# Kernel tuning notes

Measured on AMD Instinct MI355X. Metric: run time of the kernel, lower is better.

Reference implementation:

```python
import jax, jax.numpy as jnp
import numpy as np

D_EMBED = 32


def setup_inputs() -> dict:
    key = jax.random.key(0)
    ks = jax.random.split(key, 10)
    B, N, D = 16, 16384, D_EMBED
    s = 1.0 / np.sqrt(D)
    return {
        "h_pos": jax.random.normal(ks[0], (B, N, D), dtype=jnp.float32),
        "h_geo": jax.random.normal(ks[1], (B, N, D), dtype=jnp.float32),
        "n_clusters": 128,
        "Wq": jax.random.uniform(ks[2], (D, D), jnp.float32, -s, s),
        "bq": jax.random.uniform(ks[3], (D,), jnp.float32, -s, s),
        "Wk": jax.random.uniform(ks[4], (D, D), jnp.float32, -s, s),
        "bk": jax.random.uniform(ks[5], (D,), jnp.float32, -s, s),
        "Wv": jax.random.uniform(ks[6], (D, D), jnp.float32, -s, s),
        "bv": jax.random.uniform(ks[7], (D,), jnp.float32, -s, s),
        "Wo": jax.random.uniform(ks[8], (D, D), jnp.float32, -s, s),
        "bo": jax.random.uniform(ks[9], (D,), jnp.float32, -s, s),
    }


def reference(h_pos, h_geo, n_clusters, Wq, bq, Wk, bk, Wv, bv, Wo, bo):
    B, N, D = h_pos.shape
    C = n_clusters
    S = N // C  # cluster size (contiguous equal-size kmeans clusters)
    # Linear projections (torch Linear: x @ W^T + b)
    Q = h_geo @ Wq.T + bq
    K = h_geo @ Wk.T + bk
    V = h_pos @ Wv.T + bv
    # group points into clusters: [B, C, S, D]
    Qc = Q.reshape(B, C, S, D) * (1.0 / jnp.sqrt(jnp.asarray(D, Q.dtype)))
    Kc = K.reshape(B, C, S, D)
    Vc = V.reshape(B, C, S, D)
    # per-cluster attention: softmax(Q_c K_c^T) V_c
    scores = jnp.einsum("bcsd,bctd->bcst", Qc, Kc)  # [B, C, S, S]
    attn = jax.nn.softmax(scores, axis=-1)
    out = jnp.einsum("bcst,bctd->bcsd", attn, Vc).reshape(B, N, D)
    return out @ Wo.T + bo
```

## Files before the change

### kernel.cpp

```cpp
#include <hip/hip_runtime.h>

typedef __attribute__((ext_vector_type(4))) float  f32x4;
typedef __attribute__((ext_vector_type(8))) short  s16x8;

static __device__ __forceinline__ short f2bf(float x) {
    union { __bf16 b; short s; } u; u.b = (__bf16)x;
    return u.s;
}

static __device__ __forceinline__ s16x8 load_frag_f32(const float* __restrict__ base,
                                                      int stride, int row, int k0) {
    const float* p = base + (size_t)row * stride + k0;
    f32x4 a = *(const f32x4*)p;
    f32x4 b = *(const f32x4*)(p + 4);
    s16x8 f;
    f[0]=f2bf(a[0]); f[1]=f2bf(a[1]); f[2]=f2bf(a[2]); f[3]=f2bf(a[3]);
    f[4]=f2bf(b[0]); f[5]=f2bf(b[1]); f[6]=f2bf(b[2]); f[7]=f2bf(b[3]);
    return f;
}

#define MFMA(a,b,c) __builtin_amdgcn_mfma_f32_16x16x32_bf16((a),(b),(c),0,0,0)

#define GSCALE 0.25503164217809464f

__global__ __launch_bounds__(256, 3) void dlsa_kernel(
    const float* __restrict__ h_pos, const float* __restrict__ h_geo,
    const float* __restrict__ Wq, const float* __restrict__ bq,
    const float* __restrict__ Wk,
    const float* __restrict__ Wv, const float* __restrict__ bv,
    const float* __restrict__ Wo, const float* __restrict__ bo,
    float* __restrict__ out)
{
    constexpr int D = 32, S = 128, XS = 40;

    __shared__ __align__(16) short buf[20480];
    short* sVt = buf;
    short* sP  = buf + 4096;
    short* sXp = sP;
    float* cbuf = (float*)(buf + 9216);

    const int tid = threadIdx.x;
    const int wv  = tid >> 6;
    const int ln  = tid & 63;
    const int lr  = ln & 15;
    const int lg  = ln >> 4;
    const int lk  = lg << 3;
    const int r0  = wv * 32;

    short* gsl = buf + 9472 + wv * 1088;
    short* wsl = gsl + 1024;

    const f32x4 z4 = {0.f, 0.f, 0.f, 0.f};

    int cl0 = blockIdx.x * 2;
    s16x8 aXg[2], aXp[2];
    {
        const float* xg = h_geo + (size_t)cl0 * S * D;
        const float* xp = h_pos + (size_t)cl0 * S * D;
#pragma unroll
        for (int mi = 0; mi < 2; ++mi) {
            aXg[mi] = load_frag_f32(xg, D, r0 + mi * 16 + lr, lk);
            aXp[mi] = load_frag_f32(xp, D, r0 + mi * 16 + lr, lk);
        }
    }

    s16x8 aWq[2], bWk[2], a_bq;
#pragma unroll
    for (int ni = 0; ni < 2; ++ni) {
#pragma unroll
        for (int j = 0; j < 8; ++j) {
            aWq[ni][j] = f2bf(Wq[(lk + j) * 32 + ni * 16 + lr]);
            bWk[ni][j] = f2bf(Wk[(lk + j) * 32 + ni * 16 + lr]);
        }
    }
#pragma unroll
    for (int j = 0; j < 8; ++j) a_bq[j] = f2bf(bq[lk + j]);

#pragma unroll
    for (int ni = 0; ni < 2; ++ni)
#pragma unroll
        for (int kt = 0; kt < 2; ++kt) {
            f32x4 g = MFMA(aWq[ni], bWk[kt], z4);
#pragma unroll
            for (int r = 0; r < 4; ++r)
                gsl[(ni * 16 + lg * 4 + r) * 32 + kt * 16 + lr] = f2bf(g[r] * GSCALE);
        }
#pragma unroll
    for (int kt = 0; kt < 2; ++kt) {
        f32x4 w4 = MFMA(a_bq, bWk[kt], z4);
        if (lg == 0) wsl[kt * 16 + lr] = f2bf(w4[0] * GSCALE);
    }
    s16x8 fG[2];
#pragma unroll
    for (int ni = 0; ni < 2; ++ni)
        fG[ni] = *(const s16x8*)&gsl[(ni * 16 + lr) * 32 + lk];
    s16x8 wf = *(const s16x8*)&wsl[lk];
    if (lr != 0) {
#pragma unroll
        for (int i = 0; i < 8; ++i) wf[i] = 0;
    }
    s16x8 fWv[2], fWo[2];
    float vbv[2], vbo[2];
#pragma unroll
    for (int ni = 0; ni < 2; ++ni) {
        int n = ni * 16 + lr;
        fWv[ni] = load_frag_f32(Wv, 32, n, lk);
        fWo[ni] = load_frag_f32(Wo, 32, n, lk);
        vbv[ni] = bv[n]; vbo[ni] = bo[n];
    }

#pragma unroll
    for (int it = 0; it < 2; ++it) {
        float* outp = out + (size_t)(cl0 + it) * S * D;
        if (it) __syncthreads();

#pragma unroll
        for (int mi = 0; mi < 2; ++mi) {
            f32x4 cc = MFMA(aXg[mi], wf, z4);
            if (lr == 0) {
#pragma unroll
                for (int r = 0; r < 4; ++r) cbuf[r0 + mi * 16 + lg * 4 + r] = cc[r];
            }
#pragma unroll
            for (int ni = 0; ni < 2; ++ni) {
                f32x4 xq = MFMA(aXg[mi], fG[ni], z4);
                f32x4 vv = MFMA(aXp[mi], fWv[ni], z4);
                int row = r0 + mi * 16 + lg * 4;
                int col = ni * 16 + lr;
#pragma unroll
                for (int r = 0; r < 4; ++r)
                    sXp[(row + r) * XS + col] = f2bf(xq[r]);
#pragma unroll
                for (int r = 0; r < 4; ++r) {
                    int uc = lg * 4 + r;
                    int ul = wv * 2 + mi;
                    sVt[col * 128 + ((uc ^ (col & 15)) << 3) + ul] = f2bf(vv[r] + vbv[ni]);
                }
            }
        }
        __syncthreads();

        float cv[8];
#pragma unroll
        for (int nt = 0; nt < 8; ++nt) cv[nt] = cbuf[nt * 16 + lr];

        f32x4 sc[2][8];
        __builtin_amdgcn_s_setprio(1);
#pragma unroll
        for (int nt = 0; nt < 8; ++nt) {
            s16x8 xb = *(const s16x8*)&sXp[(nt * 16 + lr) * XS + lk];
            f32x4 cb = { cv[nt], cv[nt], cv[nt], cv[nt] };
            sc[0][nt] = MFMA(aXg[0], xb, cb);
            sc[1][nt] = MFMA(aXg[1], xb, cb);
        }
        __builtin_amdgcn_s_setprio(0);
        __syncthreads();

        float inv_[2][4];
#pragma unroll
        for (int mi = 0; mi < 2; ++mi) {
#pragma unroll
            for (int r = 0; r < 4; ++r) {
                float p[8]; float s = 0.f;
#pragma unroll
                for (int nt = 0; nt < 8; ++nt) {
                    p[nt] = __builtin_amdgcn_exp2f(sc[mi][nt][r]);
                    s += p[nt];
                }
                s += __shfl_xor(s, 1);
                s += __shfl_xor(s, 2);
                s += __shfl_xor(s, 4);
                s += __shfl_xor(s, 8);
                inv_[mi][r] = __builtin_amdgcn_rcpf(s);
                s16x8 pk;
#pragma unroll
                for (int nt = 0; nt < 8; ++nt) pk[nt] = f2bf(p[nt]);
                int row = r0 + mi * 16 + lg * 4 + r;
                *(s16x8*)&sP[row * 128 + ((lr ^ (row & 15)) << 3)] = pk;
            }
        }

        f32x4 ng[4], np[4];
        if (it == 0) {
            const float* xg2 = h_geo + (size_t)(cl0 + 1) * S * D;
            const float* xp2 = h_pos + (size_t)(cl0 + 1) * S * D;
#pragma unroll
            for (int mi = 0; mi < 2; ++mi) {
                const float* pg = xg2 + (size_t)(r0 + mi * 16 + lr) * D + lk;
                const float* pp = xp2 + (size_t)(r0 + mi * 16 + lr) * D + lk;
                ng[2*mi] = *(const f32x4*)pg;  ng[2*mi+1] = *(const f32x4*)(pg + 4);
                np[2*mi] = *(const f32x4*)pp;  np[2*mi+1] = *(const f32x4*)(pp + 4);
            }
        }

        f32x4 accO[2][2] = {{z4, z4}, {z4, z4}};
        __builtin_amdgcn_s_setprio(1);
#pragma unroll
        for (int kt = 0; kt < 4; ++kt) {
            int ch = kt * 4 + lg;
            s16x8 pa0 = *(const s16x8*)&sP[(r0 + lr) * 128      + ((ch ^ lr) << 3)];
            s16x8 pa1 = *(const s16x8*)&sP[(r0 + 16 + lr) * 128 + ((ch ^ lr) << 3)];
            s16x8 vb0 = *(const s16x8*)&sVt[lr * 128        + ((ch ^ lr) << 3)];
            s16x8 vb1 = *(const s16x8*)&sVt[(16 + lr) * 128 + ((ch ^ lr) << 3)];
            accO[0][0] = MFMA(pa0, vb0, accO[0][0]);
            accO[0][1] = MFMA(pa0, vb1, accO[0][1]);
            accO[1][0] = MFMA(pa1, vb0, accO[1][0]);
            accO[1][1] = MFMA(pa1, vb1, accO[1][1]);
        }
        __builtin_amdgcn_s_setprio(0);

        short* sO = sP + r0 * 128;
#pragma unroll
        for (int mi = 0; mi < 2; ++mi)
#pragma unroll
            for (int ni = 0; ni < 2; ++ni) {
                int row = mi * 16 + lg * 4;
                int col = ni * 16 + lr;
#pragma unroll
                for (int r = 0; r < 4; ++r)
                    sO[(row + r) * XS + col] = f2bf(accO[mi][ni][r] * inv_[mi][r]);
            }
        s16x8 aO0 = *(const s16x8*)&sO[lr * XS + lk];
        s16x8 aO1 = *(const s16x8*)&sO[(16 + lr) * XS + lk];

#pragma unroll
        for (int mi = 0; mi < 2; ++mi) {
            s16x8 aO = mi ? aO1 : aO0;
#pragma unroll
            for (int ni = 0; ni < 2; ++ni) {
                f32x4 y = MFMA(aO, fWo[ni], z4);
                int row = r0 + mi * 16 + lg * 4;
                int col = ni * 16 + lr;
#pragma unroll
                for (int r = 0; r < 4; ++r)
                    outp[(size_t)(row + r) * D + col] = y[r] + vbo[ni];
            }
        }

        if (it == 0) {
#pragma unroll
            for (int mi = 0; mi < 2; ++mi)
#pragma unroll
                for (int j = 0; j < 4; ++j) {
                    aXg[mi][j]     = f2bf(ng[2*mi][j]);
                    aXg[mi][4 + j] = f2bf(ng[2*mi+1][j]);
                    aXp[mi][j]     = f2bf(np[2*mi][j]);
                    aXp[mi][4 + j] = f2bf(np[2*mi+1][j]);
                }
        }
    }
}

extern "C" void kernel_launch(void* const* d_in, const int* in_sizes, int n_in,
                              void* d_out, int out_size, void* d_ws, size_t ws_size,
                              hipStream_t stream) {
    const float* h_pos = (const float*)d_in[0];
    const float* h_geo = (const float*)d_in[1];
    const float* Wq = (const float*)d_in[3];
    const float* bq = (const float*)d_in[4];
    const float* Wk = (const float*)d_in[5];
    const float* Wv = (const float*)d_in[7];
    const float* bv = (const float*)d_in[8];
    const float* Wo = (const float*)d_in[9];
    const float* bo = (const float*)d_in[10];

    dlsa_kernel<<<dim3(1024), dim3(256), 0, stream>>>(
        h_pos, h_geo, Wq, bq, Wk, Wv, bv, Wo, bo, (float*)d_out);
}
```

Before: 29.42 us.

## Assign one cluster per block with eight waves of sixteen rows

The kernel goes from 1024 blocks of 256 threads, each handling two clusters in sequence, to 2048 blocks of 512 threads, each handling a single cluster. Each of the eight waves now owns 16 query rows instead of 32. This drops the two-iteration loop and its register prefetch of the next cluster, cuts per-wave register state, and exposes more parallelism to hide latency. In exchange, the per-wave weight setup is repeated by more waves and blocks. The tighter launch bounds (512, 4) may force register spilling, and the overlap that the prefetch gave is lost.

New measurement: 37.16 us. +26.3%, slower.

```diff
diff --git a/kernel.cpp b/kernel.cpp
--- a/kernel.cpp
+++ b/kernel.cpp
@@ -23,7 +23,7 @@
 
 #define GSCALE 0.25503164217809464f
 
-__global__ __launch_bounds__(256, 3) void dlsa_kernel(
+__global__ __launch_bounds__(512, 4) void dlsa_kernel(
     const float* __restrict__ h_pos, const float* __restrict__ h_geo,
     const float* __restrict__ Wq, const float* __restrict__ bq,
     const float* __restrict__ Wk,
@@ -45,24 +45,19 @@
     const int lr  = ln & 15;
     const int lg  = ln >> 4;
     const int lk  = lg << 3;
-    const int r0  = wv * 32;
+    const int r0  = wv * 16;
 
     short* gsl = buf + 9472 + wv * 1088;
     short* wsl = gsl + 1024;
 
     const f32x4 z4 = {0.f, 0.f, 0.f, 0.f};
 
-    int cl0 = blockIdx.x * 2;
-    s16x8 aXg[2], aXp[2];
-    {
-        const float* xg = h_geo + (size_t)cl0 * S * D;
-        const float* xp = h_pos + (size_t)cl0 * S * D;
-#pragma unroll
-        for (int mi = 0; mi < 2; ++mi) {
-            aXg[mi] = load_frag_f32(xg, D, r0 + mi * 16 + lr, lk);
-            aXp[mi] = load_frag_f32(xp, D, r0 + mi * 16 + lr, lk);
-        }
-    }
+    const int cl = blockIdx.x;
+    const float* xg = h_geo + (size_t)cl * S * D;
+    const float* xp = h_pos + (size_t)cl * S * D;
+    float* outp = out + (size_t)cl * S * D;
+    s16x8 aXg = load_frag_f32(xg, D, r0 + lr, lk);
+    s16x8 aXp = load_frag_f32(xp, D, r0 + lr, lk);
 
     s16x8 aWq[2], bWk[2], a_bq;
 #pragma unroll
@@ -109,145 +104,98 @@
         vbv[ni] = bv[n]; vbo[ni] = bo[n];
     }
 
-#pragma unroll
-    for (int it = 0; it < 2; ++it) {
-        float* outp = out + (size_t)(cl0 + it) * S * D;
-        if (it) __syncthreads();
-
-#pragma unroll
-        for (int mi = 0; mi < 2; ++mi) {
-            f32x4 cc = MFMA(aXg[mi], wf, z4);
-            if (lr == 0) {
-#pragma unroll
-                for (int r = 0; r < 4; ++r) cbuf[r0 + mi * 16 + lg * 4 + r] = cc[r];
+    {
+        f32x4 cc = MFMA(aXg, wf, z4);
+        if (lr == 0) {
+#pragma unroll
+            for (int r = 0; r < 4; ++r) cbuf[r0 + lg * 4 + r] = cc[r];
+        }
+#pragma unroll
+        for (int ni = 0; ni < 2; ++ni) {
+            f32x4 xq = MFMA(aXg, fG[ni], z4);
+            f32x4 vv = MFMA(aXp, fWv[ni], z4);
+            int row = r0 + lg * 4;
+            int col = ni * 16 + lr;
+#pragma unroll
+            for (int r = 0; r < 4; ++r)
+                sXp[(row + r) * XS + col] = f2bf(xq[r]);
+#pragma unroll
+            for (int r = 0; r < 4; ++r) {
+                int uc = lg * 4 + r;
+                sVt[col * 128 + ((uc ^ (col & 15)) << 3) + wv] = f2bf(vv[r] + vbv[ni]);
             }
-#pragma unroll
-            for (int ni = 0; ni < 2; ++ni) {
-                f32x4 xq = MFMA(aXg[mi], fG[ni], z4);
-                f32x4 vv = MFMA(aXp[mi], fWv[ni], z4);
-                int row = r0 + mi * 16 + lg * 4;
-                int col = ni * 16 + lr;
-#pragma unroll
-                for (int r = 0; r < 4; ++r)
-                    sXp[(row + r) * XS + col] = f2bf(xq[r]);
-#pragma unroll
-                for (int r = 0; r < 4; ++r) {
-                    int uc = lg * 4 + r;
-                    int ul = wv * 2 + mi;
-                    sVt[col * 128 + ((uc ^ (col & 15)) << 3) + ul] = f2bf(vv[r] + vbv[ni]);
-                }
-            }
-        }
-        __syncthreads();
-
-        float cv[8];
-#pragma unroll
-        for (int nt = 0; nt < 8; ++nt) cv[nt] = cbuf[nt * 16 + lr];
-
-        f32x4 sc[2][8];
-        __builtin_amdgcn_s_setprio(1);
+        }
+    }
+    __syncthreads();
+
+    float cv[8];
+#pragma unroll
+    for (int nt = 0; nt < 8; ++nt) cv[nt] = cbuf[nt * 16 + lr];
+
+    f32x4 sc[8];
+    __builtin_amdgcn_s_setprio(1);
+#pragma unroll
+    for (int nt = 0; nt < 8; ++nt) {
+        s16x8 xb = *(const s16x8*)&sXp[(nt * 16 + lr) * XS + lk];
+        f32x4 cb = { cv[nt], cv[nt], cv[nt], cv[nt] };
+        sc[nt] = MFMA(aXg, xb, cb);
+    }
+    __builtin_amdgcn_s_setprio(0);
+    __syncthreads();
+
+    float inv_[4];
+#pragma unroll
+    for (int r = 0; r < 4; ++r) {
+        float p[8]; float s = 0.f;
 #pragma unroll
         for (int nt = 0; nt < 8; ++nt) {
-            s16x8 xb = *(const s16x8*)&sXp[(nt * 16 + lr) * XS + lk];
-            f32x4 cb = { cv[nt], cv[nt], cv[nt], cv[nt] };
-            sc[0][nt] = MFMA(aXg[0], xb, cb);
-            sc[1][nt] = MFMA(aXg[1], xb, cb);
-        }
-        __builtin_amdgcn_s_setprio(0);
-        __syncthreads();
-
-        float inv_[2][4];
-#pragma unroll
-        for (int mi = 0; mi < 2; ++mi) {
-#pragma unroll
-            for (int r = 0; r < 4; ++r) {
-                float p[8]; float s = 0.f;
-#pragma unroll
-                for (int nt = 0; nt < 8; ++nt) {
-                    p[nt] = __builtin_amdgcn_exp2f(sc[mi][nt][r]);
-                    s += p[nt];
-                }
-                s += __shfl_xor(s, 1);
-                s += __shfl_xor(s, 2);
-                s += __shfl_xor(s, 4);
-                s += __shfl_xor(s, 8);
-                inv_[mi][r] = __builtin_amdgcn_rcpf(s);
-                s16x8 pk;
-#pragma unroll
-                for (int nt = 0; nt < 8; ++nt) pk[nt] = f2bf(p[nt]);
-                int row = r0 + mi * 16 + lg * 4 + r;
-                *(s16x8*)&sP[row * 128 + ((lr ^ (row & 15)) << 3)] = pk;
-            }
-        }
-
-        f32x4 ng[4], np[4];
-        if (it == 0) {
-            const float* xg2 = h_geo + (size_t)(cl0 + 1) * S * D;
-            const float* xp2 = h_pos + (size_t)(cl0 + 1) * S * D;
-#pragma unroll
-            for (int mi = 0; mi < 2; ++mi) {
-                const float* pg = xg2 + (size_t)(r0 + mi * 16 + lr) * D + lk;
-                const float* pp = xp2 + (size_t)(r0 + mi * 16 + lr) * D + lk;
-                ng[2*mi] = *(const f32x4*)pg;  ng[2*mi+1] = *(const f32x4*)(pg + 4);
-                np[2*mi] = *(const f32x4*)pp;  np[2*mi+1] = *(const f32x4*)(pp + 4);
-            }
-        }
-
-        f32x4 accO[2][2] = {{z4, z4}, {z4, z4}};
-        __builtin_amdgcn_s_setprio(1);
-#pragma unroll
-        for (int kt = 0; kt < 4; ++kt) {
-            int ch = kt * 4 + lg;
-            s16x8 pa0 = *(const s16x8*)&sP[(r0 + lr) * 128      + ((ch ^ lr) << 3)];
-            s16x8 pa1 = *(const s16x8*)&sP[(r0 + 16 + lr) * 128 + ((ch ^ lr) << 3)];
-            s16x8 vb0 = *(const s16x8*)&sVt[lr * 128        + ((ch ^ lr) << 3)];
-            s16x8 vb1 = *(const s16x8*)&sVt[(16 + lr) * 128 + ((ch ^ lr) << 3)];
-            accO[0][0] = MFMA(pa0, vb0, accO[0][0]);
-            accO[0][1] = MFMA(pa0, vb1, accO[0][1]);
-            accO[1][0] = MFMA(pa1, vb0, accO[1][0]);
-            accO[1][1] = MFMA(pa1, vb1, accO[1][1]);
-        }
-        __builtin_amdgcn_s_setprio(0);
-
-        short* sO = sP + r0 * 128;
-#pragma unroll
-        for (int mi = 0; mi < 2; ++mi)
-#pragma unroll
-            for (int ni = 0; ni < 2; ++ni) {
-                int row = mi * 16 + lg * 4;
-                int col = ni * 16 + lr;
-#pragma unroll
-                for (int r = 0; r < 4; ++r)
-                    sO[(row + r) * XS + col] = f2bf(accO[mi][ni][r] * inv_[mi][r]);
-            }
-        s16x8 aO0 = *(const s16x8*)&sO[lr * XS + lk];
-        s16x8 aO1 = *(const s16x8*)&sO[(16 + lr) * XS + lk];
-
-#pragma unroll
-        for (int mi = 0; mi < 2; ++mi) {
-            s16x8 aO = mi ? aO1 : aO0;
-#pragma unroll
-            for (int ni = 0; ni < 2; ++ni) {
-                f32x4 y = MFMA(aO, fWo[ni], z4);
-                int row = r0 + mi * 16 + lg * 4;
-                int col = ni * 16 + lr;
-#pragma unroll
-                for (int r = 0; r < 4; ++r)
-                    outp[(size_t)(row + r) * D + col] = y[r] + vbo[ni];
-            }
-        }
-
-        if (it == 0) {
-#pragma unroll
-            for (int mi = 0; mi < 2; ++mi)
-#pragma unroll
-                for (int j = 0; j < 4; ++j) {
-                    aXg[mi][j]     = f2bf(ng[2*mi][j]);
-                    aXg[mi][4 + j] = f2bf(ng[2*mi+1][j]);
-                    aXp[mi][j]     = f2bf(np[2*mi][j]);
-                    aXp[mi][4 + j] = f2bf(np[2*mi+1][j]);
-                }
-        }
+            p[nt] = __builtin_amdgcn_exp2f(sc[nt][r]);
+            s += p[nt];
+        }
+        s += __shfl_xor(s, 1);
+        s += __shfl_xor(s, 2);
+        s += __shfl_xor(s, 4);
+        s += __shfl_xor(s, 8);
+        inv_[r] = __builtin_amdgcn_rcpf(s);
+        s16x8 pk;
+#pragma unroll
+        for (int nt = 0; nt < 8; ++nt) pk[nt] = f2bf(p[nt]);
+        int row = r0 + lg * 4 + r;
+        *(s16x8*)&sP[row * 128 + ((lr ^ (row & 15)) << 3)] = pk;
+    }
+
+    f32x4 accO[2] = {z4, z4};
+    __builtin_amdgcn_s_setprio(1);
+#pragma unroll
+    for (int kt = 0; kt < 4; ++kt) {
+        int ch = kt * 4 + lg;
+        s16x8 pa  = *(const s16x8*)&sP[(r0 + lr) * 128 + ((ch ^ lr) << 3)];
+        s16x8 vb0 = *(const s16x8*)&sVt[lr * 128        + ((ch ^ lr) << 3)];
+        s16x8 vb1 = *(const s16x8*)&sVt[(16 + lr) * 128 + ((ch ^ lr) << 3)];
+        accO[0] = MFMA(pa, vb0, accO[0]);
+        accO[1] = MFMA(pa, vb1, accO[1]);
+    }
+    __builtin_amdgcn_s_setprio(0);
+
+    short* sO = sP + r0 * 128;
+#pragma unroll
+    for (int ni = 0; ni < 2; ++ni) {
+        int row = lg * 4;
+        int col = ni * 16 + lr;
+#pragma unroll
+        for (int r = 0; r < 4; ++r)
+            sO[(row + r) * XS + col] = f2bf(accO[ni][r] * inv_[r]);
+    }
+    s16x8 aO = *(const s16x8*)&sO[lr * XS + lk];
+
+#pragma unroll
+    for (int ni = 0; ni < 2; ++ni) {
+        f32x4 y = MFMA(aO, fWo[ni], z4);
+        int row = r0 + lg * 4;
+        int col = ni * 16 + lr;
+#pragma unroll
+        for (int r = 0; r < 4; ++r)
+            outp[(size_t)(row + r) * D + col] = y[r] + vbo[ni];
     }
 }
 
@@ -264,6 +212,6 @@
     const float* Wo = (const float*)d_in[9];
     const float* bo = (const float*)d_in[10];
 
-    dlsa_kernel<<<dim3(1024), dim3(256), 0, stream>>>(
+    dlsa_kernel<<<dim3(2048), dim3(512), 0, stream>>>(
         h_pos, h_geo, Wq, bq, Wk, Wv, bv, Wo, bo, (float*)d_out);
 }
```
